# Kernel optimization log

Hardware: AMD Instinct MI355X
Metric: run time of the kernel (lower is better)

The kernel has to match this reference:

```python
import jax, jax.numpy as jnp
import numpy as np
from jax import lax

N = 2048          # batch_size*2 (two views)
DIM_IN = 1024     # stub encoder input width
DIM_FEAT = 2048
DIM = 128
C = 1000          # num_classes
Q = 8             # queue_size_per_cls
K_POS = 4         # select_num_pos
K_NEG = 1024      # select_num_neg
EPS = 1e-5


def setup_inputs() -> dict:
    key = jax.random.key(0)
    ks = jax.random.split(key, 12)
    img = jax.random.normal(ks[0], (N, DIM_IN), dtype=jnp.float32)
    labels = jax.random.randint(ks[1], (N,), 0, C)
    # buffers
    ql = jax.random.normal(ks[2], (DIM, Q * C), dtype=jnp.float32)
    queue_list = ql / jnp.linalg.norm(ql, axis=0, keepdims=True)
    queue_ptr = jnp.zeros((C,), dtype=jnp.int32)
    pos_index = jnp.asarray(np.arange(Q * C).reshape(C, Q))
    cols = np.arange(Q * (C - 1))
    # skip class-i block: indices >= Q*i shift up by Q
    neg_index = jnp.asarray(cols[None, :] + Q * ((cols[None, :] // Q) >= np.arange(C)[:, None]))
    # params (stub encoder + mlp head + classifier)
    s = 0.02
    enc_W = s * jax.random.normal(ks[3], (DIM_IN, DIM_FEAT), dtype=jnp.float32)
    enc_b = jnp.zeros((DIM_FEAT,), dtype=jnp.float32)
    mlp_W1 = s * jax.random.normal(ks[4], (DIM_FEAT, DIM_FEAT), dtype=jnp.float32)
    mlp_b1 = jnp.zeros((DIM_FEAT,), dtype=jnp.float32)
    bn_gamma = jnp.ones((DIM_FEAT,), dtype=jnp.float32)
    bn_beta = jnp.zeros((DIM_FEAT,), dtype=jnp.float32)
    mlp_W2 = s * jax.random.normal(ks[5], (DIM_FEAT, DIM), dtype=jnp.float32)
    mlp_b2 = jnp.zeros((DIM,), dtype=jnp.float32)
    lin_W = s * jax.random.normal(ks[6], (DIM_FEAT, C), dtype=jnp.float32)
    lin_b = jnp.zeros((C,), dtype=jnp.float32)
    return dict(img=img, labels=labels, queue_list=queue_list, queue_ptr=queue_ptr,
                pos_index=pos_index, neg_index=neg_index,
                enc_W=enc_W, enc_b=enc_b, mlp_W1=mlp_W1, mlp_b1=mlp_b1,
                bn_gamma=bn_gamma, bn_beta=bn_beta, mlp_W2=mlp_W2, mlp_b2=mlp_b2,
                lin_W=lin_W, lin_b=lin_b)


def _offdiag_idx(n):
    # idx[i,j] = j + (j >= i): gather columns of an [n,n] matrix skipping the diagonal
    cols = jnp.arange(n - 1)
    return cols[None, :] + (cols[None, :] >= jnp.arange(n)[:, None]).astype(cols.dtype)


def reference(img, labels, queue_list, queue_ptr, pos_index, neg_index,
              enc_W, enc_b, mlp_W1, mlp_b1, bn_gamma, bn_beta,
              mlp_W2, mlp_b2, lin_W, lin_b):
    # encoder (stub) -> mid_feat
    mid = img @ enc_W + enc_b                                  # [N, DIM_FEAT]
    # mlp: Linear -> BatchNorm1d (training stats) -> ReLU -> Linear
    h = mid @ mlp_W1 + mlp_b1
    mu = jnp.mean(h, axis=0)
    var = jnp.var(h, axis=0)
    h = (h - mu) * lax.rsqrt(var + EPS) * bn_gamma + bn_beta
    h = jax.nn.relu(h)
    feat = h @ mlp_W2 + mlp_b2
    feat = feat / jnp.linalg.norm(feat, axis=1, keepdims=True)  # [N, DIM]
    logit_cls = mid @ lin_W + lin_b                             # [N, C]

    # queue similarities (queue is detached in the original)
    ql = lax.stop_gradient(queue_list)
    sim_q = feat @ ql                                           # [N, Q*C]
    sim_pos = jnp.take_along_axis(sim_q, pos_index[labels], axis=1)   # [N, Q]
    sim_neg = jnp.take_along_axis(sim_q, neg_index[labels], axis=1)   # [N, Q*(C-1)]
    pos_sel = -lax.top_k(-sim_pos, K_POS)[0]     # hardest (smallest) positives
    neg_sel = lax.top_k(sim_neg, K_NEG)[0]       # hardest (largest) negatives

    # in-batch similarities with diagonal removed
    sim_b = feat @ feat.T                                       # [N, N]
    off = _offdiag_idx(sim_b.shape[0])
    sim_b_off = jnp.take_along_axis(sim_b, off, axis=1)         # [N, N-1]
    sim_con = jnp.concatenate([sim_b_off, pos_sel, neg_sel], axis=1)

    lab_b = (labels[:, None] == labels[None, :]).astype(jnp.float32)
    lab_off = jnp.take_along_axis(lab_b, off, axis=1)
    labels_con = jnp.concatenate([lab_off, jnp.ones_like(pos_sel), jnp.zeros_like(neg_sel)], axis=1)

    # dequeue/enqueue: sequential per-sample scatter into per-class circular buffer
    feat_k = lax.stop_gradient(feat[: feat.shape[0] // 2])
    labels_k = labels[: labels.shape[0] // 2]

    def step(carry, x):
        ql_, qp_ = carry
        f, c = x
        ptr = qp_[c]
        real = c * Q + ptr
        ql_ = ql_.at[:, real].set(f)
        qp_ = qp_.at[c].set((ptr + 1) % Q)
        return (ql_, qp_), None

    (queue_list_new, queue_ptr_new), _ = lax.scan(step, (queue_list, queue_ptr), (feat_k, labels_k))
    return sim_con, labels_con, logit_cls, queue_list_new, queue_ptr_new
```

## Files before the change

kernel.cpp:

```cpp
#include <hip/hip_runtime.h>
#include <cstdint>
#include <cstddef>

#define NB      2048
#define DIN     1024
#define DF      2048
#define DM      128
#define NCLS    1000
#define QQ      8
#define QC      8000
#define QCP     8064
#define CONW    3075
#define FSPLIT  8
#define NBUCK   8192

using float4v = __attribute__((ext_vector_type(4))) float;
using bf16x8  = __attribute__((ext_vector_type(8))) __bf16;

#define GLB_AS __attribute__((address_space(1)))
#define LDS_AS __attribute__((address_space(3)))

__device__ __forceinline__ unsigned short f2bf(float f) {
  unsigned int u = __float_as_uint(f);
  u += 0x7fffu + ((u >> 16) & 1u);
  return (unsigned short)(u >> 16);
}
__device__ __forceinline__ float bf2f(unsigned short u) {
  return __uint_as_float(((unsigned int)u) << 16);
}

__device__ __forceinline__ bf16x8 ld_frag8(const unsigned short* p) {
  union { uint4 u; bf16x8 b; } cv;
  cv.u = *(const uint4*)p;
  return cv.b;
}

__device__ __forceinline__ void gload_lds16(const unsigned short* g, unsigned short* l) {
  __builtin_amdgcn_global_load_lds((const GLB_AS unsigned int*)g,
                                   (LDS_AS unsigned int*)l, 16, 0, 0);
}

__global__ void conv_bf16_kernel(const float* __restrict__ in, unsigned short* __restrict__ out, int n) {
  int idx = blockIdx.x * 256 + threadIdx.x;
  if (idx < n) out[idx] = f2bf(in[idx]);
}

struct TDescs {
  const float* src[5];
  unsigned short* dst[5];
  int K[5], N[5], nx[5], ky[5];
};
__global__ void transpose_all_kernel(TDescs d) {
  const int mid = blockIdx.y;
  const int nx = d.nx[mid];
  const int kb32 = blockIdx.x / nx, nb32 = blockIdx.x % nx;
  if (kb32 >= d.ky[mid]) return;
  const float* src = d.src[mid];
  unsigned short* dst = d.dst[mid];
  const int K = d.K[mid], N = d.N[mid];
  const int nb = nb32 * 32, kb = kb32 * 32;
  __shared__ float tile[32][33];
  int tx = threadIdx.x, ty = threadIdx.y;
#pragma unroll
  for (int r = 0; r < 32; r += 8) {
    int k = kb + ty + r, n = nb + tx;
    tile[ty + r][tx] = (n < N) ? src[(size_t)k * N + n] : 0.f;
  }
  __syncthreads();
#pragma unroll
  for (int r = 0; r < 32; r += 8) {
    int n = nb + ty + r, k = kb + tx;
    dst[(size_t)n * K + k] = f2bf(tile[tx][ty + r]);
  }
}

template<int OUT_MODE, bool HAS_BIAS, bool BN_STATS>
__global__ __launch_bounds__(256) void gemm_bt_kernel(
    const unsigned short* __restrict__ A,
    const unsigned short* __restrict__ Bt,
    const float* __restrict__ bias,
    void* __restrict__ Cout,
    int lda, int kbeg, int klen, int ldc, int n_store,
    float* __restrict__ ps, float* __restrict__ ps2)
{
  __shared__ __align__(16) unsigned short As[2][128][32];
  __shared__ __align__(16) unsigned short Bs[2][64][32];
  const int m0 = blockIdx.y * 128, n0 = blockIdx.x * 64;
  const int z  = blockIdx.z;
  const int tid = threadIdx.x;
  const int lane = tid & 63, w = tid >> 6;
  const int wm = (w >> 1) * 64, wn = (w & 1) * 32;
  const int lrow = lane & 15, lq = lane >> 4;

  const int kb = kbeg + z * klen;
  const unsigned short* Abase = A  + (size_t)m0 * lda + kb;
  const unsigned short* Bbase = Bt + (size_t)n0 * lda + kb;

  const int c0 = tid, c1 = tid + 256;
  const size_t a_off0 = (size_t)(c0 >> 2) * lda + (c0 & 3) * 8;
  const size_t a_off1 = (size_t)(c1 >> 2) * lda + (c1 & 3) * 8;
  const size_t b_off  = (size_t)(tid >> 2) * lda + (tid & 3) * 8;

  float4v acc[4][2];
#pragma unroll
  for (int i = 0; i < 4; ++i)
#pragma unroll
    for (int j = 0; j < 2; ++j)
      acc[i][j] = (float4v){0.f, 0.f, 0.f, 0.f};

  auto stage = [&](int buf, int k0) {
    gload_lds16(Abase + a_off0 + k0, &As[buf][0][0] + c0 * 8);
    gload_lds16(Abase + a_off1 + k0, &As[buf][0][0] + c1 * 8);
    gload_lds16(Bbase + b_off  + k0, &Bs[buf][0][0] + tid * 8);
  };

  const int NKT = klen / 32;
  stage(0, 0);
  for (int t = 0; t < NKT; ++t) {
    __syncthreads();
    if (t + 1 < NKT) stage((t + 1) & 1, (t + 1) * 32);
    const int b = t & 1;
    bf16x8 af[4], bfr[2];
#pragma unroll
    for (int i = 0; i < 4; ++i) af[i]  = ld_frag8(&As[b][wm + i * 16 + lrow][lq * 8]);
#pragma unroll
    for (int j = 0; j < 2; ++j) bfr[j] = ld_frag8(&Bs[b][wn + j * 16 + lrow][lq * 8]);
#pragma unroll
    for (int i = 0; i < 4; ++i)
#pragma unroll
      for (int j = 0; j < 2; ++j)
        acc[i][j] = __builtin_amdgcn_mfma_f32_16x16x32_bf16(af[i], bfr[j], acc[i][j], 0, 0, 0);
  }

  float* cs  = (float*)&As[0][0][0];
  float* cs2 = cs + 64;
  if (BN_STATS) {
    __syncthreads();
    if (tid < 128) cs[tid] = 0.f;
    __syncthreads();
  }

  float*          outf = (float*)Cout          + (size_t)z * NB * ldc;
  unsigned short* outh = (unsigned short*)Cout + (size_t)z * NB * ldc;

#pragma unroll
  for (int j = 0; j < 2; ++j) {
    int gcol = n0 + wn + j * 16 + lrow;
    float bv = 0.f;
    if (HAS_BIAS && gcol < n_store) bv = bias[gcol];
    float sj = 0.f, s2j = 0.f;
#pragma unroll
    for (int i = 0; i < 4; ++i) {
#pragma unroll
      for (int r = 0; r < 4; ++r) {
        int grow = m0 + wm + i * 16 + lq * 4 + r;
        float val = acc[i][j][r] + bv;
        if (BN_STATS) { sj += val; s2j += val * val; }
        if (OUT_MODE == 0) {
          if (gcol < n_store) outf[(size_t)grow * ldc + gcol] = val;
        } else if (OUT_MODE == 1) {
          if (gcol < n_store) outh[(size_t)grow * ldc + gcol] = f2bf(val);
        } else {
          if (gcol != grow) outf[(size_t)grow * ldc + gcol - (gcol > grow)] = val;
        }
      }
    }
    if (BN_STATS) {
      atomicAdd(&cs [wn + j * 16 + lrow], sj);
      atomicAdd(&cs2[wn + j * 16 + lrow], s2j);
    }
  }
  if (BN_STATS) {
    __syncthreads();
    if (tid < 64) {
      ps [(size_t)blockIdx.y * DF + n0 + tid] = cs[tid];
      ps2[(size_t)blockIdx.y * DF + n0 + tid] = cs2[tid];
    }
  }
}

__global__ void bn_finish_kernel(const float* __restrict__ ps, const float* __restrict__ ps2,
                                 const float* __restrict__ gamma, const float* __restrict__ beta,
                                 float* __restrict__ scale, float* __restrict__ bias) {
  int j = blockIdx.x * 256 + threadIdx.x;
  float s = 0.f, s2 = 0.f;
  for (int b = 0; b < 16; ++b) { s += ps[b * DF + j]; s2 += ps2[b * DF + j]; }
  float mu  = s  * (1.f / NB);
  float var = s2 * (1.f / NB) - mu * mu;
  float sc = gamma[j] * rsqrtf(var + 1e-5f);
  scale[j] = sc;
  bias[j]  = beta[j] - mu * sc;
}

__global__ void bn_apply_kernel(const float* __restrict__ h, const float* __restrict__ scale,
                                const float* __restrict__ bias, unsigned short* __restrict__ hb) {
  size_t idx = (size_t)blockIdx.x * 256 + threadIdx.x;
  int j = (int)(idx & (DF - 1));
  float v = h[idx] * scale[j] + bias[j];
  v = fmaxf(v, 0.f);
  hb[idx] = f2bf(v);
}

__global__ void feat_reduce_norm_kernel(const float* __restrict__ part, const float* __restrict__ b2,
                                        float* __restrict__ fo, unsigned short* __restrict__ fb) {
  int row = blockIdx.x, t = threadIdx.x;
  float v0 = b2[t], v1 = b2[64 + t];
#pragma unroll
  for (int s = 0; s < FSPLIT; ++s) {
    const float* p = part + (size_t)s * NB * DM + (size_t)row * DM;
    v0 += p[t]; v1 += p[64 + t];
  }
  float ss = v0 * v0 + v1 * v1;
#pragma unroll
  for (int o = 32; o > 0; o >>= 1) ss += __shfl_xor(ss, o);
  float inv = rsqrtf(ss);
  v0 *= inv; v1 *= inv;
  fo[row * DM + t] = v0;       fo[row * DM + 64 + t] = v1;
  fb[row * DM + t] = f2bf(v0); fb[row * DM + 64 + t] = f2bf(v1);
}

__global__ __launch_bounds__(256) void topk_kernel(const unsigned short* __restrict__ sim_qb,
                                                   const int* __restrict__ labels,
                                                   float* __restrict__ out_simcon) {
  __shared__ unsigned int hist[NBUCK];
  __shared__ float sbuf[1024];
  __shared__ unsigned int wtot[4];
  __shared__ int s_tb;

  const int row = blockIdx.x;
  const int c = labels[row];
  const int t = threadIdx.x;
  const int w = t >> 6, lane = t & 63;

  uint4* h4 = (uint4*)hist;
  uint4 z4; z4.x = z4.y = z4.z = z4.w = 0u;
#pragma unroll
  for (int i = 0; i < 8; ++i) h4[t + 256 * i] = z4;

  float vals[32];
  float pvals[QQ];
  const unsigned short* rp = sim_qb + (size_t)row * QC;
#pragma unroll
  for (int j = 0; j < 4; ++j) {
    const int cls = j * 256 + t;
    uint4 u4 = *(const uint4*)(rp + j * 2048 + t * 8);
    const unsigned int uu[4] = {u4.x, u4.y, u4.z, u4.w};
    const bool masked = (cls >= NCLS) || (cls == c);
#pragma unroll
    for (int e = 0; e < 4; ++e) {
      float lo = bf2f((unsigned short)(uu[e] & 0xffffu));
      float hi = bf2f((unsigned short)(uu[e] >> 16));
      if (cls == c) { pvals[2 * e] = lo; pvals[2 * e + 1] = hi; }
      vals[j * 8 + 2 * e]     = masked ? -4.f : lo;
      vals[j * 8 + 2 * e + 1] = masked ? -4.f : hi;
    }
  }
  __syncthreads();

#pragma unroll
  for (int i = 0; i < 32; ++i) {
    float v = vals[i];
    if (v > -3.f) {
      int b = (int)((v + 1.0f) * 4096.0f);
      b = min(max(b, 0), NBUCK - 1);
      atomicAdd(&hist[b], 1u);
    }
  }
  __syncthreads();

  unsigned int cnt[32];
#pragma unroll
  for (int k = 0; k < 8; ++k) {
    uint4 u = h4[t * 8 + k];
    cnt[4 * k] = u.x; cnt[4 * k + 1] = u.y; cnt[4 * k + 2] = u.z; cnt[4 * k + 3] = u.w;
  }
  unsigned int chunktot = 0;
#pragma unroll
  for (int i = 0; i < 32; ++i) chunktot += cnt[i];

  unsigned int s = chunktot;
#pragma unroll
  for (int off = 1; off < 64; off <<= 1) {
    unsigned int v = __shfl_down(s, off);
    if (lane + off < 64) s += v;
  }
  if (lane == 0) wtot[w] = s;
  __syncthreads();
  unsigned int wsfx = 0;
#pragma unroll
  for (int ww = 0; ww < 4; ++ww) if (ww > w) wsfx += wtot[ww];
  unsigned int S = wsfx + s - chunktot;

  unsigned int ofsv[32];
#pragma unroll
  for (int i = 31; i >= 0; --i) {
    unsigned int cb = cnt[i];
    ofsv[i] = S;
    unsigned int Sincl = S + cb;
    if (S < 1024u && Sincl >= 1024u) s_tb = t * 32 + i;
    S = Sincl;
  }
#pragma unroll
  for (int k = 0; k < 8; ++k) {
    uint4 u;
    u.x = ofsv[4 * k]; u.y = ofsv[4 * k + 1]; u.z = ofsv[4 * k + 2]; u.w = ofsv[4 * k + 3];
    h4[t * 8 + k] = u;
  }
  __syncthreads();

  const int tb = s_tb;
#pragma unroll
  for (int i = 0; i < 32; ++i) {
    float v = vals[i];
    if (v > -3.f) {
      int b = (int)((v + 1.0f) * 4096.0f);
      b = min(max(b, 0), NBUCK - 1);
      if (b >= tb) {
        unsigned int p = atomicAdd(&hist[b], 1u);
        if (p < 1024u) sbuf[p] = v;
      }
    }
  }
  __syncthreads();

  float* orow = out_simcon + (size_t)row * CONW;
  for (int idx = t; idx < 1024; idx += 256) orow[2051 + idx] = sbuf[idx];
  if (t == (c & 255) && (c >> 8) < 4 && (c >> 8) * 256 + t == c) {
    for (int a2 = 1; a2 < QQ; ++a2) {
      float key = pvals[a2]; int b2 = a2 - 1;
      while (b2 >= 0 && pvals[b2] > key) { pvals[b2 + 1] = pvals[b2]; --b2; }
      pvals[b2 + 1] = key;
    }
#pragma unroll
    for (int s2 = 0; s2 < 4; ++s2) orow[2047 + s2] = pvals[s2];
  }
}

__global__ void labels_con_kernel(const int* __restrict__ labels, float* __restrict__ out_lab) {
  int i = blockIdx.x;
  int li = labels[i];
  for (int j = threadIdx.x; j < CONW; j += 256) {
    float v;
    if (j < NB - 1)      v = (labels[j + (j >= i)] == li) ? 1.f : 0.f;
    else if (j < NB + 3) v = 1.f;
    else                 v = 0.f;
    out_lab[(size_t)i * CONW + j] = v;
  }
}

__global__ void queue_scan_kernel(const int* __restrict__ labels, const int* __restrict__ qptr_in,
                                  int* __restrict__ writer, float* __restrict__ qptr_out) {
  __shared__ int wloc[QQ];
  const int c = blockIdx.x;
  const int lane = threadIdx.x;
  if (lane < QQ) wloc[lane] = -1;
  __syncthreads();
  const int p0 = qptr_in[c];
  int cnt = 0;
#pragma unroll
  for (int t = 0; t < (NB / 2) / 64; ++t) {
    int i = t * 64 + lane;
    bool pred = (labels[i] == c);
    unsigned long long mask = __ballot(pred);
    if (pred) {
      int rank = __popcll(mask & ((1ull << lane) - 1ull));
      int slot = (p0 + cnt + rank) & (QQ - 1);
      atomicMax(&wloc[slot], i);
    }
    cnt += __popcll(mask);
  }
  __syncthreads();
  if (lane < QQ) writer[c * QQ + lane] = wloc[lane];
  if (lane == 0) qptr_out[c] = (float)((p0 + cnt) & (QQ - 1));
}

__global__ void queue_write_kernel(const int* __restrict__ writer, const float* __restrict__ feat,
                                   const float* __restrict__ qin, float* __restrict__ qout) {
  int idx = blockIdx.x * 256 + threadIdx.x;
  int col = idx % QC;
  int d   = idx / QC;
  int wsrc = writer[col];
  float v = (wsrc >= 0) ? feat[(size_t)wsrc * DM + d] : qin[idx];
  qout[idx] = v;
}

extern "C" void kernel_launch(void* const* d_in, const int* in_sizes, int n_in,
                              void* d_out, int out_size, void* d_ws, size_t ws_size,
                              hipStream_t stream) {
  const float* img     = (const float*)d_in[0];
  const int*   labels  = (const int*)  d_in[1];
  const float* queue_l = (const float*)d_in[2];
  const int*   queue_p = (const int*)  d_in[3];
  const float* enc_W   = (const float*)d_in[6];
  const float* enc_b   = (const float*)d_in[7];
  const float* W1      = (const float*)d_in[8];
  const float* b1      = (const float*)d_in[9];
  const float* gamma   = (const float*)d_in[10];
  const float* beta    = (const float*)d_in[11];
  const float* W2      = (const float*)d_in[12];
  const float* b2      = (const float*)d_in[13];
  const float* linW    = (const float*)d_in[14];
  const float* linb    = (const float*)d_in[15];

  float* out        = (float*)d_out;
  float* out_simcon = out;
  float* out_labcon = out + (size_t)NB * CONW;
  float* out_logit  = out + (size_t)2 * NB * CONW;
  float* out_qlist  = out_logit + (size_t)NB * NCLS;
  float* out_qptr   = out_qlist + (size_t)DM * QC;

  char* wsp = (char*)d_ws;
  size_t off = 0;
  auto alloc = [&](size_t bytes) -> void* {
    void* p = wsp + off;
    off += (bytes + 255) & ~(size_t)255;
    return p;
  };
  unsigned short* img_bf  = (unsigned short*)alloc((size_t)NB * DIN * 2);
  unsigned short* encWt   = (unsigned short*)alloc((size_t)DF * DIN * 2);
  unsigned short* W1t     = (unsigned short*)alloc((size_t)DF * DF * 2);
  unsigned short* W2t     = (unsigned short*)alloc((size_t)DM * DF * 2);
  unsigned short* linWt   = (unsigned short*)alloc((size_t)1024 * DF * 2);
  unsigned short* qlt     = (unsigned short*)alloc((size_t)QCP * DM * 2);
  unsigned short* mid_bf  = (unsigned short*)alloc((size_t)NB * DF * 2);
  float*          h_pre   = (float*)alloc((size_t)NB * DF * 4);
  unsigned short* h_bf    = (unsigned short*)alloc((size_t)NB * DF * 2);
  float*          part_s  = (float*)alloc((size_t)16 * DF * 4);
  float*          part_s2 = (float*)alloc((size_t)16 * DF * 4);
  float*          bn_sc   = (float*)alloc((size_t)DF * 4);
  float*          bn_bi   = (float*)alloc((size_t)DF * 4);
  float*          feat_part=(float*)alloc((size_t)FSPLIT * NB * DM * 4);
  float*          feat_f  = (float*)alloc((size_t)NB * DM * 4);
  unsigned short* feat_bf = (unsigned short*)alloc((size_t)NB * DM * 2);
  unsigned short* sim_qb  = (unsigned short*)alloc((size_t)NB * QC * 2 + 512);
  int*            writer  = (int*)alloc((size_t)QC * 4);

  dim3 blk256(256);
  dim3 tblk(32, 8);

  conv_bf16_kernel<<<dim3((NB * DIN) / 256), blk256, 0, stream>>>(img, img_bf, NB * DIN);
  TDescs td;
  td.src[0] = enc_W;  td.dst[0] = encWt; td.K[0] = DIN; td.N[0] = DF;   td.nx[0] = DF / 32;   td.ky[0] = DIN / 32;
  td.src[1] = W1;     td.dst[1] = W1t;   td.K[1] = DF;  td.N[1] = DF;   td.nx[1] = DF / 32;   td.ky[1] = DF / 32;
  td.src[2] = W2;     td.dst[2] = W2t;   td.K[2] = DF;  td.N[2] = DM;   td.nx[2] = DM / 32;   td.ky[2] = DF / 32;
  td.src[3] = linW;   td.dst[3] = linWt; td.K[3] = DF;  td.N[3] = NCLS; td.nx[3] = 1024 / 32; td.ky[3] = DF / 32;
  td.src[4] = queue_l;td.dst[4] = qlt;   td.K[4] = DM;  td.N[4] = QC;   td.nx[4] = QCP / 32;  td.ky[4] = DM / 32;
  transpose_all_kernel<<<dim3(4096, 5), tblk, 0, stream>>>(td);

  gemm_bt_kernel<1, true, false><<<dim3(DF / 64, NB / 128), blk256, 0, stream>>>(
      img_bf, encWt, enc_b, mid_bf, DIN, 0, DIN, DF, DF, nullptr, nullptr);

  gemm_bt_kernel<0, true, true><<<dim3(DF / 64, NB / 128), blk256, 0, stream>>>(
      mid_bf, W1t, b1, h_pre, DF, 0, DF, DF, DF, part_s, part_s2);

  bn_finish_kernel<<<dim3(DF / 256), blk256, 0, stream>>>(part_s, part_s2, gamma, beta, bn_sc, bn_bi);
  bn_apply_kernel<<<dim3((NB * DF) / 256), blk256, 0, stream>>>(h_pre, bn_sc, bn_bi, h_bf);

  gemm_bt_kernel<0, false, false><<<dim3(DM / 64, NB / 128, FSPLIT), blk256, 0, stream>>>(
      h_bf, W2t, nullptr, feat_part, DF, 0, DF / FSPLIT, DM, DM, nullptr, nullptr);

  feat_reduce_norm_kernel<<<dim3(NB), dim3(64), 0, stream>>>(feat_part, b2, feat_f, feat_bf);

  gemm_bt_kernel<0, true, false><<<dim3(1024 / 64, NB / 128), blk256, 0, stream>>>(
      mid_bf, linWt, linb, out_logit, DF, 0, DF, NCLS, NCLS, nullptr, nullptr);

  gemm_bt_kernel<1, false, false><<<dim3(QCP / 64, NB / 128), blk256, 0, stream>>>(
      feat_bf, qlt, nullptr, sim_qb, DM, 0, DM, QC, QC, nullptr, nullptr);

  gemm_bt_kernel<2, false, false><<<dim3(NB / 64, NB / 128), blk256, 0, stream>>>(
      feat_bf, feat_bf, nullptr, out_simcon, DM, 0, DM, CONW, NB, nullptr, nullptr);

  topk_kernel<<<dim3(NB), blk256, 0, stream>>>(sim_qb, labels, out_simcon);

  labels_con_kernel<<<dim3(NB), blk256, 0, stream>>>(labels, out_labcon);

  queue_scan_kernel<<<dim3(NCLS), dim3(64), 0, stream>>>(labels, queue_p, writer, out_qptr);
  queue_write_kernel<<<dim3((DM * QC) / 256), blk256, 0, stream>>>(writer, feat_f, queue_l, out_qlist);
}
```

Baseline: 342.7 us.

## Fuse W1 and classifier GEMMs, fuse queue and in-batch sim GEMMs, bf16 pre-BN

Places linWt directly after W1t, and feat_bf directly after qlt, so each pair of B matrices that share an A operand forms one contiguous buffer. This lets the W1 GEMM and the classifier-logit GEMM run as one launch, and the queue-similarity GEMM and the in-batch similarity GEMM run as another, with the output mode chosen per column block. The pre-BN activation is now stored as bf16 instead of fp32, and bn_apply is vectorised to process 8 elements per thread, which halves that intermediate's traffic. The fused launches depend on the exact workspace layout for contiguity, and storing pre-BN values in bf16 adds rounding before normalisation.

```diff
diff --git a/kernel.cpp b/kernel.cpp
--- a/kernel.cpp
+++ b/kernel.cpp
@@ -10,6 +10,7 @@
 #define QQ      8
 #define QC      8000
 #define QCP     8064
+#define NLP     1024
 #define CONW    3075
 #define FSPLIT  8
 #define NBUCK   8192
@@ -79,8 +80,10 @@
     const unsigned short* __restrict__ A,
     const unsigned short* __restrict__ Bt,
     const float* __restrict__ bias,
+    const float* __restrict__ bias2,
     void* __restrict__ Cout,
-    int lda, int kbeg, int klen, int ldc, int n_store,
+    void* __restrict__ Cout2,
+    int lda, int klen, int ldc, int n_store,
     float* __restrict__ ps, float* __restrict__ ps2)
 {
   __shared__ __align__(16) unsigned short As[2][128][32];
@@ -92,9 +95,8 @@
   const int wm = (w >> 1) * 64, wn = (w & 1) * 32;
   const int lrow = lane & 15, lq = lane >> 4;
 
-  const int kb = kbeg + z * klen;
-  const unsigned short* Abase = A  + (size_t)m0 * lda + kb;
-  const unsigned short* Bbase = Bt + (size_t)n0 * lda + kb;
+  const unsigned short* Abase = A  + (size_t)m0 * lda + z * klen;
+  const unsigned short* Bbase = Bt + (size_t)n0 * lda + z * klen;
 
   const int c0 = tid, c1 = tid + 256;
   const size_t a_off0 = (size_t)(c0 >> 2) * lda + (c0 & 3) * 8;
@@ -132,22 +134,29 @@
         acc[i][j] = __builtin_amdgcn_mfma_f32_16x16x32_bf16(af[i], bfr[j], acc[i][j], 0, 0, 0);
   }
 
+  const bool is2nd = (OUT_MODE == 3 && n0 >= DF) || (OUT_MODE == 4 && n0 >= QCP);
+  const bool do_bn = BN_STATS && !is2nd;
+
   float* cs  = (float*)&As[0][0][0];
   float* cs2 = cs + 64;
-  if (BN_STATS) {
+  if (do_bn) {
     __syncthreads();
     if (tid < 128) cs[tid] = 0.f;
     __syncthreads();
   }
 
-  float*          outf = (float*)Cout          + (size_t)z * NB * ldc;
-  unsigned short* outh = (unsigned short*)Cout + (size_t)z * NB * ldc;
+  float*          outf  = (float*)Cout          + (size_t)z * NB * ldc;
+  unsigned short* outh  = (unsigned short*)Cout + (size_t)z * NB * ldc;
+  float*          outf2 = (float*)Cout2;
 
 #pragma unroll
   for (int j = 0; j < 2; ++j) {
     int gcol = n0 + wn + j * 16 + lrow;
     float bv = 0.f;
-    if (HAS_BIAS && gcol < n_store) bv = bias[gcol];
+    if (OUT_MODE == 3) {
+      if (!is2nd) bv = bias[gcol];
+      else if (gcol - DF < NCLS) bv = bias2[gcol - DF];
+    } else if (HAS_BIAS && gcol < n_store) bv = bias[gcol];
     float sj = 0.f, s2j = 0.f;
 #pragma unroll
     for (int i = 0; i < 4; ++i) {
@@ -155,22 +164,29 @@
       for (int r = 0; r < 4; ++r) {
         int grow = m0 + wm + i * 16 + lq * 4 + r;
         float val = acc[i][j][r] + bv;
-        if (BN_STATS) { sj += val; s2j += val * val; }
+        if (do_bn) { sj += val; s2j += val * val; }
         if (OUT_MODE == 0) {
           if (gcol < n_store) outf[(size_t)grow * ldc + gcol] = val;
         } else if (OUT_MODE == 1) {
           if (gcol < n_store) outh[(size_t)grow * ldc + gcol] = f2bf(val);
-        } else {
-          if (gcol != grow) outf[(size_t)grow * ldc + gcol - (gcol > grow)] = val;
+        } else if (OUT_MODE == 3) {
+          if (!is2nd) outh[(size_t)grow * DF + gcol] = f2bf(val);
+          else if (gcol - DF < NCLS) outf2[(size_t)grow * NCLS + (gcol - DF)] = val;
+        } else if (OUT_MODE == 4) {
+          if (!is2nd) { if (gcol < QC) outh[(size_t)grow * QC + gcol] = f2bf(val); }
+          else {
+            int gc2 = gcol - QCP;
+            if (gc2 != grow) outf2[(size_t)grow * CONW + gc2 - (gc2 > grow)] = val;
+          }
         }
       }
     }
-    if (BN_STATS) {
+    if (do_bn) {
       atomicAdd(&cs [wn + j * 16 + lrow], sj);
       atomicAdd(&cs2[wn + j * 16 + lrow], s2j);
     }
   }
-  if (BN_STATS) {
+  if (do_bn) {
     __syncthreads();
     if (tid < 64) {
       ps [(size_t)blockIdx.y * DF + n0 + tid] = cs[tid];
@@ -192,13 +208,24 @@
   bias[j]  = beta[j] - mu * sc;
 }
 
-__global__ void bn_apply_kernel(const float* __restrict__ h, const float* __restrict__ scale,
+__global__ void bn_apply_kernel(const unsigned short* __restrict__ h, const float* __restrict__ scale,
                                 const float* __restrict__ bias, unsigned short* __restrict__ hb) {
-  size_t idx = (size_t)blockIdx.x * 256 + threadIdx.x;
-  int j = (int)(idx & (DF - 1));
-  float v = h[idx] * scale[j] + bias[j];
-  v = fmaxf(v, 0.f);
-  hb[idx] = f2bf(v);
+  int base = (blockIdx.x * 256 + threadIdx.x) * 8;
+  int j = base & (DF - 1);
+  uint4 u = *(const uint4*)(h + base);
+  unsigned int uu[4] = {u.x, u.y, u.z, u.w};
+  unsigned int rr[4];
+#pragma unroll
+  for (int e = 0; e < 4; ++e) {
+    int col = j + 2 * e;
+    float lo = bf2f((unsigned short)(uu[e] & 0xffffu));
+    float hi = bf2f((unsigned short)(uu[e] >> 16));
+    lo = fmaxf(lo * scale[col] + bias[col], 0.f);
+    hi = fmaxf(hi * scale[col + 1] + bias[col + 1], 0.f);
+    rr[e] = (unsigned int)f2bf(lo) | ((unsigned int)f2bf(hi) << 16);
+  }
+  uint4 o; o.x = rr[0]; o.y = rr[1]; o.z = rr[2]; o.w = rr[3];
+  *(uint4*)(hb + base) = o;
 }
 
 __global__ void feat_reduce_norm_kernel(const float* __restrict__ part, const float* __restrict__ b2,
@@ -419,11 +446,12 @@
   unsigned short* img_bf  = (unsigned short*)alloc((size_t)NB * DIN * 2);
   unsigned short* encWt   = (unsigned short*)alloc((size_t)DF * DIN * 2);
   unsigned short* W1t     = (unsigned short*)alloc((size_t)DF * DF * 2);
+  unsigned short* linWt   = (unsigned short*)alloc((size_t)NLP * DF * 2);
   unsigned short* W2t     = (unsigned short*)alloc((size_t)DM * DF * 2);
-  unsigned short* linWt   = (unsigned short*)alloc((size_t)1024 * DF * 2);
   unsigned short* qlt     = (unsigned short*)alloc((size_t)QCP * DM * 2);
+  unsigned short* feat_bf = (unsigned short*)alloc((size_t)NB * DM * 2);
   unsigned short* mid_bf  = (unsigned short*)alloc((size_t)NB * DF * 2);
-  float*          h_pre   = (float*)alloc((size_t)NB * DF * 4);
+  unsigned short* h_pbf   = (unsigned short*)alloc((size_t)NB * DF * 2);
   unsigned short* h_bf    = (unsigned short*)alloc((size_t)NB * DF * 2);
   float*          part_s  = (float*)alloc((size_t)16 * DF * 4);
   float*          part_s2 = (float*)alloc((size_t)16 * DF * 4);
@@ -431,7 +459,6 @@
   float*          bn_bi   = (float*)alloc((size_t)DF * 4);
   float*          feat_part=(float*)alloc((size_t)FSPLIT * NB * DM * 4);
   float*          feat_f  = (float*)alloc((size_t)NB * DM * 4);
-  unsigned short* feat_bf = (unsigned short*)alloc((size_t)NB * DM * 2);
   unsigned short* sim_qb  = (unsigned short*)alloc((size_t)NB * QC * 2 + 512);
   int*            writer  = (int*)alloc((size_t)QC * 4);
 
@@ -443,32 +470,26 @@
   td.src[0] = enc_W;  td.dst[0] = encWt; td.K[0] = DIN; td.N[0] = DF;   td.nx[0] = DF / 32;   td.ky[0] = DIN / 32;
   td.src[1] = W1;     td.dst[1] = W1t;   td.K[1] = DF;  td.N[1] = DF;   td.nx[1] = DF / 32;   td.ky[1] = DF / 32;
   td.src[2] = W2;     td.dst[2] = W2t;   td.K[2] = DF;  td.N[2] = DM;   td.nx[2] = DM / 32;   td.ky[2] = DF / 32;
-  td.src[3] = linW;   td.dst[3] = linWt; td.K[3] = DF;  td.N[3] = NCLS; td.nx[3] = 1024 / 32; td.ky[3] = DF / 32;
+  td.src[3] = linW;   td.dst[3] = linWt; td.K[3] = DF;  td.N[3] = NCLS; td.nx[3] = NLP / 32;  td.ky[3] = DF / 32;
   td.src[4] = queue_l;td.dst[4] = qlt;   td.K[4] = DM;  td.N[4] = QC;   td.nx[4] = QCP / 32;  td.ky[4] = DM / 32;
   transpose_all_kernel<<<dim3(4096, 5), tblk, 0, stream>>>(td);
 
   gemm_bt_kernel<1, true, false><<<dim3(DF / 64, NB / 128), blk256, 0, stream>>>(
-      img_bf, encWt, enc_b, mid_bf, DIN, 0, DIN, DF, DF, nullptr, nullptr);
-
-  gemm_bt_kernel<0, true, true><<<dim3(DF / 64, NB / 128), blk256, 0, stream>>>(
-      mid_bf, W1t, b1, h_pre, DF, 0, DF, DF, DF, part_s, part_s2);
+      img_bf, encWt, enc_b, nullptr, mid_bf, nullptr, DIN, DIN, DF, DF, nullptr, nullptr);
+
+  gemm_bt_kernel<3, true, true><<<dim3((DF + NLP) / 64, NB / 128), blk256, 0, stream>>>(
+      mid_bf, W1t, b1, linb, h_pbf, out_logit, DF, DF, DF, DF, part_s, part_s2);
 
   bn_finish_kernel<<<dim3(DF / 256), blk256, 0, stream>>>(part_s, part_s2, gamma, beta, bn_sc, bn_bi);
-  bn_apply_kernel<<<dim3((NB * DF) / 256), blk256, 0, stream>>>(h_pre, bn_sc, bn_bi, h_bf);
+  bn_apply_kernel<<<dim3((NB * DF) / 2048), blk256, 0, stream>>>(h_pbf, bn_sc, bn_bi, h_bf);
 
   gemm_bt_kernel<0, false, false><<<dim3(DM / 64, NB / 128, FSPLIT), blk256, 0, stream>>>(
-      h_bf, W2t, nullptr, feat_part, DF, 0, DF / FSPLIT, DM, DM, nullptr, nullptr);
+      h_bf, W2t, nullptr, nullptr, feat_part, nullptr, DF, DF / FSPLIT, DM, DM, nullptr, nullptr);
 
   feat_reduce_norm_kernel<<<dim3(NB), dim3(64), 0, stream>>>(feat_part, b2, feat_f, feat_bf);
 
-  gemm_bt_kernel<0, true, false><<<dim3(1024 / 64, NB / 128), blk256, 0, stream>>>(
-      mid_bf, linWt, linb, out_logit, DF, 0, DF, NCLS, NCLS, nullptr, nullptr);
-
-  gemm_bt_kernel<1, false, false><<<dim3(QCP / 64, NB / 128), blk256, 0, stream>>>(
-      feat_bf, qlt, nullptr, sim_qb, DM, 0, DM, QC, QC, nullptr, nullptr);
-
-  gemm_bt_kernel<2, false, false><<<dim3(NB / 64, NB / 128), blk256, 0, stream>>>(
-      feat_bf, feat_bf, nullptr, out_simcon, DM, 0, DM, CONW, NB, nullptr, nullptr);
+  gemm_bt_kernel<4, false, false><<<dim3((QCP + NB) / 64, NB / 128), blk256, 0, stream>>>(
+      feat_bf, qlt, nullptr, nullptr, sim_qb, out_simcon, DM, DM, QC, QC, nullptr, nullptr);
 
   topk_kernel<<<dim3(NB), blk256, 0, stream>>>(sim_qb, labels, out_simcon);
 
```

New measurement: 319.6 us. 1.07x faster.
